# Kernel tuning notes

Measured on AMD Instinct MI355X. Metric: run time of the kernel, lower is better.

Reference implementation:

```python
import jax, jax.numpy as jnp
import numpy as np

B, N, E, F, OUT = 2, 50000, 150000, 256, 256

def setup_inputs() -> dict:
    key = jax.random.key(0)
    ks = jax.random.split(key, 8)
    X = jax.random.normal(ks[0], (B, N, F), dtype=jnp.float32)
    e = jax.random.uniform(ks[1], (B, E), dtype=jnp.float32)
    ri_idx = jax.random.randint(ks[2], (B, E), 0, N, dtype=jnp.int32)
    ro_idx = jax.random.randint(ks[3], (B, E), 0, N, dtype=jnp.int32)
    W1 = jax.random.normal(ks[4], (3 * F, OUT), dtype=jnp.float32) * (1.0 / np.sqrt(3 * F))
    b1 = jnp.zeros((OUT,), dtype=jnp.float32)
    W2 = jax.random.normal(ks[5], (OUT, OUT), dtype=jnp.float32) * (1.0 / np.sqrt(OUT))
    b2 = jnp.zeros((OUT,), dtype=jnp.float32)
    return {"X": X, "e": e, "ri_idx": ri_idx, "ro_idx": ro_idx,
            "W1": W1, "b1": b1, "W2": W2, "b2": b2}


def _aggregate(x, ew, ri, ro):
    # x: [N,F], ew: [E], ri/ro: [E] receiver/sender node ids per edge.
    # bi = Ri^T X = x[ri]; bo = Ro^T X = x[ro]
    # mi = Ri diag(e) bo : scatter-add weighted sender feats to receivers
    # mo = Ro diag(e) bi : scatter-add weighted receiver feats to senders
    n = x.shape[0]
    w = ew[:, None]
    mi = jax.ops.segment_sum(w * x[ro], ri, num_segments=n)
    mo = jax.ops.segment_sum(w * x[ri], ro, num_segments=n)
    return mi, mo


def reference(X, e, ri_idx, ro_idx, W1, b1, W2, b2):
    mi, mo = jax.vmap(_aggregate)(X, e, ri_idx, ro_idx)   # each [B,N,F]
    M = jnp.concatenate([mi, mo, X], axis=2)              # [B,N,3F]
    h = jnp.tanh(M @ W1 + b1)
    return jnp.tanh(h @ W2 + b2)
```

## Files before the change

### kernel.cpp

```cpp
#include <hip/hip_runtime.h>
#include <hip/hip_bf16.h>
#include <cstdint>
#include <cstddef>

#define BATCH 2
#define NNODE 50000
#define NEDGE 150000
#define FDIM 256
#define MTOT (BATCH * NNODE)
#define NSEG (2 * BATCH * NNODE)
#define NEDG2 (2 * BATCH * NEDGE)
#define SCAN_NB 98

typedef __attribute__((ext_vector_type(8))) __bf16 bf16x8;
typedef __attribute__((ext_vector_type(4))) float f32x4;

__device__ __forceinline__ ushort f32_to_bf16_rne(float x) {
    uint32_t u = __builtin_bit_cast(uint32_t, x);
    u = (u + 0x7fffu + ((u >> 16) & 1u)) >> 16;
    return (ushort)u;
}

__device__ __forceinline__ void split2(float x, ushort& h, ushort& l) {
    h = f32_to_bf16_rne(x);
    float hf = __builtin_bit_cast(float, ((uint32_t)h) << 16);
    l = f32_to_bf16_rne(x - hf);
}

__global__ __launch_bounds__(256)
void prep_kernel(const float* __restrict__ W1, const float* __restrict__ W2,
                 ushort* __restrict__ W1h, ushort* __restrict__ W1l,
                 ushort* __restrict__ W2h, ushort* __restrict__ W2l) {
    int idx = blockIdx.x * 256 + threadIdx.x;
    if (idx < 768 * 256) {
        int k = idx >> 8, n = idx & 255;
        ushort h, l;
        split2(W1[idx], h, l);
        W1h[n * 768 + k] = h;
        W1l[n * 768 + k] = l;
    }
    if (idx < 256 * 256) {
        int k = idx >> 8, n = idx & 255;
        ushort h, l;
        split2(W2[idx], h, l);
        W2h[n * 256 + k] = h;
        W2l[n * 256 + k] = l;
    }
}

__global__ __launch_bounds__(256)
void hist_kernel(const int* __restrict__ ri, const int* __restrict__ ro,
                 int* __restrict__ cnt) {
    int j = blockIdx.x * 256 + threadIdx.x;
    if (j >= BATCH * NEDGE) return;
    int b = j / NEDGE;
    atomicAdd(&cnt[(0 * BATCH + b) * NNODE + ri[j]], 1);
    atomicAdd(&cnt[(1 * BATCH + b) * NNODE + ro[j]], 1);
}

__global__ __launch_bounds__(256)
void scan1_kernel(const int* __restrict__ cnt, int* __restrict__ rs,
                  int* __restrict__ bsum) {
    __shared__ int s[256];
    int tid = threadIdx.x;
    int base = blockIdx.x * 2048 + tid * 8;
    int v[8];
    int loc = 0;
#pragma unroll
    for (int j = 0; j < 8; ++j) {
        int idx = base + j;
        int x = (idx < NSEG) ? cnt[idx] : 0;
        v[j] = x;
        loc += x;
    }
    s[tid] = loc;
    __syncthreads();
    for (int off = 1; off < 256; off <<= 1) {
        int t = (tid >= off) ? s[tid - off] : 0;
        __syncthreads();
        s[tid] += t;
        __syncthreads();
    }
    int run = (tid == 0) ? 0 : s[tid - 1];
#pragma unroll
    for (int j = 0; j < 8; ++j) {
        int idx = base + j;
        if (idx < NSEG) rs[idx] = run;
        run += v[j];
    }
    if (tid == 255) bsum[blockIdx.x] = s[255];
}

__global__ __launch_bounds__(128)
void scan2_kernel(int* __restrict__ bsum) {
    __shared__ int s[128];
    int tid = threadIdx.x;
    int x = (tid < SCAN_NB) ? bsum[tid] : 0;
    s[tid] = x;
    __syncthreads();
    for (int off = 1; off < 128; off <<= 1) {
        int t = (tid >= off) ? s[tid - off] : 0;
        __syncthreads();
        s[tid] += t;
        __syncthreads();
    }
    int ex = (tid == 0) ? 0 : s[tid - 1];
    if (tid < SCAN_NB) bsum[tid] = ex;
}

__global__ __launch_bounds__(256)
void scan3_kernel(int* __restrict__ rs, int* __restrict__ cur,
                  const int* __restrict__ bsum) {
    int base = blockIdx.x * 2048 + threadIdx.x * 8;
    int off = bsum[blockIdx.x];
#pragma unroll
    for (int j = 0; j < 8; ++j) {
        int idx = base + j;
        if (idx < NSEG) {
            int v = rs[idx] + off;
            rs[idx] = v;
            cur[idx] = v;
        }
    }
}

__global__ __launch_bounds__(256)
void fill_kernel(const int* __restrict__ ri, const int* __restrict__ ro,
                 const float* __restrict__ e, int* __restrict__ cur,
                 int* __restrict__ pidx, float* __restrict__ pw) {
    int j = blockIdx.x * 256 + threadIdx.x;
    if (j >= BATCH * NEDGE) return;
    int b = j / NEDGE;
    int vri = ri[j], vro = ro[j];
    float ew = e[j];
    int p0 = atomicAdd(&cur[(0 * BATCH + b) * NNODE + vri], 1);
    pidx[p0] = vro;
    pw[p0] = ew;
    int p1 = atomicAdd(&cur[(1 * BATCH + b) * NNODE + vro], 1);
    pidx[p1] = vri;
    pw[p1] = ew;
}

__global__ __launch_bounds__(256)
void gather_kernel(const float* __restrict__ X, const int* __restrict__ rs,
                   const int* __restrict__ cnt, const int* __restrict__ pidx,
                   const float* __restrict__ pw,
                   float* __restrict__ mi, float* __restrict__ mo) {
    int gid = blockIdx.x * 256 + threadIdx.x;
    int w = gid >> 6;
    int lane = gid & 63;
    if (w >= NSEG) return;
    int t = w / (BATCH * NNODE);
    int r = w - t * (BATCH * NNODE);
    int b = r / NNODE;
    int start = rs[w];
    int c = cnt[w];
    const float* Xb = X + (size_t)b * NNODE * FDIM;
    float4 acc = make_float4(0.f, 0.f, 0.f, 0.f);
    for (int i = 0; i < c; ++i) {
        int v = pidx[start + i];
        float ww = pw[start + i];
        float4 xv = *(const float4*)(Xb + (size_t)v * FDIM + lane * 4);
        acc.x += ww * xv.x;
        acc.y += ww * xv.y;
        acc.z += ww * xv.z;
        acc.w += ww * xv.w;
    }
    float* dst = (t == 0 ? mi : mo) + (size_t)r * FDIM + lane * 4;
    *(float4*)dst = acc;
}

template<int KTOT, bool SECOND>
__global__ __launch_bounds__(256, 2)
void gemm_kernel(const float* __restrict__ A0, const float* __restrict__ A1,
                 const float* __restrict__ A2,
                 const ushort* __restrict__ Bhg, const ushort* __restrict__ Blg,
                 const float* __restrict__ bias,
                 uint32_t* __restrict__ hout, float* __restrict__ fout) {
    __shared__ ushort Ah[128][36], Al[128][36], Bh[128][36], Bl[128][36];

    int tid = threadIdx.x;
    int lane = tid & 63;
    int wid = tid >> 6;
    int wm = wid >> 1, wn = wid & 1;
    int r0 = blockIdx.x * 128;
    int c0 = blockIdx.y * 128;

    f32x4 acc[4][4];
    f32x4 zero4 = {0.f, 0.f, 0.f, 0.f};
#pragma unroll
    for (int m = 0; m < 4; ++m)
#pragma unroll
        for (int n = 0; n < 4; ++n) acc[m][n] = zero4;

    for (int k0 = 0; k0 < KTOT; k0 += 32) {
        {
            int c4 = (tid & 7) * 4;
            int rr = tid >> 3;
            if constexpr (!SECOND) {
                const float* src;
                int kb;
                if (k0 < 256)      { src = A0; kb = k0; }
                else if (k0 < 512) { src = A1; kb = k0 - 256; }
                else               { src = A2; kb = k0 - 512; }
#pragma unroll
                for (int it = 0; it < 4; ++it) {
                    int row = it * 32 + rr;
                    int rg = r0 + row;
                    float4 v = make_float4(0.f, 0.f, 0.f, 0.f);
                    if (rg < MTOT) v = *(const float4*)(src + (size_t)rg * 256 + kb + c4);
                    ushort h0, l0, h1, l1, h2, l2, h3, l3;
                    split2(v.x, h0, l0); split2(v.y, h1, l1);
                    split2(v.z, h2, l2); split2(v.w, h3, l3);
                    *(ushort4*)&Ah[row][c4] = make_ushort4(h0, h1, h2, h3);
                    *(ushort4*)&Al[row][c4] = make_ushort4(l0, l1, l2, l3);
                }
            } else {
                const uint32_t* src = (const uint32_t*)A0;
#pragma unroll
                for (int it = 0; it < 4; ++it) {
                    int row = it * 32 + rr;
                    int rg = r0 + row;
                    uint4 v = make_uint4(0u, 0u, 0u, 0u);
                    if (rg < MTOT) v = *(const uint4*)(src + (size_t)rg * 256 + k0 + c4);
                    *(ushort4*)&Ah[row][c4] = make_ushort4((ushort)v.x, (ushort)v.y,
                                                           (ushort)v.z, (ushort)v.w);
                    *(ushort4*)&Al[row][c4] = make_ushort4((ushort)(v.x >> 16), (ushort)(v.y >> 16),
                                                           (ushort)(v.z >> 16), (ushort)(v.w >> 16));
                }
            }
        }
        {
            int i = tid & 127;
            int seg = (tid >> 7) * 16;
            const ushort* gh = Bhg + (size_t)(c0 + i) * KTOT + k0 + seg;
            const ushort* gl = Blg + (size_t)(c0 + i) * KTOT + k0 + seg;
#pragma unroll
            for (int j = 0; j < 2; ++j) {
                *(uint4*)&Bh[i][seg + j * 8] = *(const uint4*)(gh + j * 8);
                *(uint4*)&Bl[i][seg + j * 8] = *(const uint4*)(gl + j * 8);
            }
        }
        __syncthreads();

        {
            int ko = (lane >> 4) * 8;
            bf16x8 ah[4], al[4], bh[4], bl[4];
#pragma unroll
            for (int m = 0; m < 4; ++m) {
                int row = wm * 64 + m * 16 + (lane & 15);
                ah[m] = *(const bf16x8*)&Ah[row][ko];
                al[m] = *(const bf16x8*)&Al[row][ko];
            }
#pragma unroll
            for (int n = 0; n < 4; ++n) {
                int coln = wn * 64 + n * 16 + (lane & 15);
                bh[n] = *(const bf16x8*)&Bh[coln][ko];
                bl[n] = *(const bf16x8*)&Bl[coln][ko];
            }
#pragma unroll
            for (int m = 0; m < 4; ++m)
#pragma unroll
                for (int n = 0; n < 4; ++n) {
                    acc[m][n] = __builtin_amdgcn_mfma_f32_16x16x32_bf16(ah[m], bh[n], acc[m][n], 0, 0, 0);
                    acc[m][n] = __builtin_amdgcn_mfma_f32_16x16x32_bf16(al[m], bh[n], acc[m][n], 0, 0, 0);
                    acc[m][n] = __builtin_amdgcn_mfma_f32_16x16x32_bf16(ah[m], bl[n], acc[m][n], 0, 0, 0);
                }
        }
        __syncthreads();
    }

#pragma unroll
    for (int m = 0; m < 4; ++m) {
        int rbase = r0 + wm * 64 + m * 16 + ((lane >> 4) * 4);
#pragma unroll
        for (int n = 0; n < 4; ++n) {
            int col = c0 + wn * 64 + n * 16 + (lane & 15);
            float bv = bias[col];
#pragma unroll
            for (int q = 0; q < 4; ++q) {
                int row = rbase + q;
                if (row < MTOT) {
                    float t = tanhf(acc[m][n][q] + bv);
                    if constexpr (!SECOND) {
                        ushort h, l;
                        split2(t, h, l);
                        hout[(size_t)row * 256 + col] = (uint32_t)h | ((uint32_t)l << 16);
                    } else {
                        fout[(size_t)row * 256 + col] = t;
                    }
                }
            }
        }
    }
}

extern "C" void kernel_launch(void* const* d_in, const int* in_sizes, int n_in,
                              void* d_out, int out_size, void* d_ws, size_t ws_size,
                              hipStream_t stream) {
    const float* X  = (const float*)d_in[0];
    const float* e  = (const float*)d_in[1];
    const int*   ri = (const int*)d_in[2];
    const int*   ro = (const int*)d_in[3];
    const float* W1 = (const float*)d_in[4];
    const float* b1 = (const float*)d_in[5];
    const float* W2 = (const float*)d_in[6];
    const float* b2 = (const float*)d_in[7];
    float* out = (float*)d_out;

    char* ws = (char*)d_ws;
    const size_t szMI = (size_t)MTOT * 256 * 4;
    float*    mi   = (float*)ws;
    float*    mo   = (float*)(ws + szMI);
    char*     hreg = ws + 2 * szMI;
    uint32_t* hbuf = (uint32_t*)hreg;
    ushort*   W1h  = (ushort*)(ws + 3 * szMI);
    ushort*   W1l  = W1h + 768 * 256;
    ushort*   W2h  = W1l + 768 * 256;
    ushort*   W2l  = W2h + 256 * 256;

    int*   cnt  = (int*)(hreg);
    int*   rs   = (int*)(hreg + 800000);
    int*   cur  = (int*)(hreg + 1600000);
    int*   bsum = (int*)(hreg + 2400000);
    int*   pidx = (int*)(hreg + 2404096);
    float* pw   = (float*)(hreg + 4804096);

    hipMemsetAsync(cnt, 0, (size_t)NSEG * 4, stream);

    prep_kernel<<<768, 256, 0, stream>>>(W1, W2, W1h, W1l, W2h, W2l);

    hist_kernel<<<(BATCH * NEDGE + 255) / 256, 256, 0, stream>>>(ri, ro, cnt);
    scan1_kernel<<<SCAN_NB, 256, 0, stream>>>(cnt, rs, bsum);
    scan2_kernel<<<1, 128, 0, stream>>>(bsum);
    scan3_kernel<<<SCAN_NB, 256, 0, stream>>>(rs, cur, bsum);
    fill_kernel<<<(BATCH * NEDGE + 255) / 256, 256, 0, stream>>>(ri, ro, e, cur, pidx, pw);

    gather_kernel<<<NSEG / 4, 256, 0, stream>>>(X, rs, cnt, pidx, pw, mi, mo);

    dim3 grid1((MTOT + 127) / 128, 2);
    gemm_kernel<768, false><<<grid1, 256, 0, stream>>>(
        mi, mo, X, W1h, W1l, b1, hbuf, nullptr);

    gemm_kernel<256, true><<<grid1, 256, 0, stream>>>(
        (const float*)hbuf, nullptr, nullptr, W2h, W2l, b2, nullptr, out);
}
```

Before: 827.1 us.

## Double-buffer GEMM tiles via direct global-to-LDS loads with swizzled weight images

The GEMM kernels now stage A and B tiles straight into LDS with global_load_lds into a 64KB double buffer, prefetching the next K-tile while MFMAs run on the current one. The bf16 hi/lo split of A moves from the staging step to the fragment-read step, and the weights are pre-split into a swizzled tile-major image so B loads are contiguous and LDS reads avoid bank conflicts. The gather loop is also unrolled by two to keep more loads in flight. In exchange, each block uses much more LDS, which may cut occupancy, and the split work is repeated for each wave column.

```diff
diff --git a/kernel.cpp b/kernel.cpp
--- a/kernel.cpp
+++ b/kernel.cpp
@@ -9,11 +9,15 @@
 #define FDIM 256
 #define MTOT (BATCH * NNODE)
 #define NSEG (2 * BATCH * NNODE)
-#define NEDG2 (2 * BATCH * NEDGE)
 #define SCAN_NB 98
 
 typedef __attribute__((ext_vector_type(8))) __bf16 bf16x8;
+typedef __attribute__((ext_vector_type(8))) ushort u16x8;
 typedef __attribute__((ext_vector_type(4))) float f32x4;
+typedef __attribute__((ext_vector_type(4))) uint32_t u32x4;
+
+typedef const __attribute__((address_space(1))) uint32_t* gptr_t;
+typedef __attribute__((address_space(3))) uint32_t* lptr_t;
 
 __device__ __forceinline__ ushort f32_to_bf16_rne(float x) {
     uint32_t u = __builtin_bit_cast(uint32_t, x);
@@ -29,22 +33,40 @@
 
 __global__ __launch_bounds__(256)
 void prep_kernel(const float* __restrict__ W1, const float* __restrict__ W2,
-                 ushort* __restrict__ W1h, ushort* __restrict__ W1l,
-                 ushort* __restrict__ W2h, ushort* __restrict__ W2l) {
+                 ushort* __restrict__ i1h, ushort* __restrict__ i1l,
+                 ushort* __restrict__ i2h, ushort* __restrict__ i2l) {
     int idx = blockIdx.x * 256 + threadIdx.x;
-    if (idx < 768 * 256) {
-        int k = idx >> 8, n = idx & 255;
-        ushort h, l;
-        split2(W1[idx], h, l);
-        W1h[n * 768 + k] = h;
-        W1l[n * 768 + k] = l;
-    }
-    if (idx < 256 * 256) {
-        int k = idx >> 8, n = idx & 255;
-        ushort h, l;
-        split2(W2[idx], h, l);
-        W2h[n * 256 + k] = h;
-        W2l[n * 256 + k] = l;
+    if (idx < 24576) {
+        int kb = idx >> 10;
+        int col = (idx >> 2) & 255;
+        int s = idx & 3;
+        int cb = col >> 7, c = col & 127;
+        int sw = s ^ ((c >> 1) & 3);
+        ushort hs[8], ls[8];
+#pragma unroll
+        for (int j = 0; j < 8; ++j) {
+            int k = kb * 32 + sw * 8 + j;
+            split2(W1[(size_t)k * 256 + col], hs[j], ls[j]);
+        }
+        size_t off = ((size_t)(kb * 2 + cb) * 128 + c) * 32 + s * 8;
+#pragma unroll
+        for (int j = 0; j < 8; ++j) { i1h[off + j] = hs[j]; i1l[off + j] = ls[j]; }
+    }
+    if (idx < 8192) {
+        int kb = idx >> 10;
+        int col = (idx >> 2) & 255;
+        int s = idx & 3;
+        int cb = col >> 7, c = col & 127;
+        int sw = s ^ ((c >> 1) & 3);
+        ushort hs[8], ls[8];
+#pragma unroll
+        for (int j = 0; j < 8; ++j) {
+            int k = kb * 32 + sw * 8 + j;
+            split2(W2[(size_t)k * 256 + col], hs[j], ls[j]);
+        }
+        size_t off = ((size_t)(kb * 2 + cb) * 128 + c) * 32 + s * 8;
+#pragma unroll
+        for (int j = 0; j < 8; ++j) { i2h[off + j] = hs[j]; i2l[off + j] = ls[j]; }
     }
 }
 
@@ -155,36 +177,49 @@
     int b = r / NNODE;
     int start = rs[w];
     int c = cnt[w];
-    const float* Xb = X + (size_t)b * NNODE * FDIM;
+    int end = start + c;
+    const float* Xb = X + (size_t)b * NNODE * FDIM + lane * 4;
     float4 acc = make_float4(0.f, 0.f, 0.f, 0.f);
-    for (int i = 0; i < c; ++i) {
-        int v = pidx[start + i];
-        float ww = pw[start + i];
-        float4 xv = *(const float4*)(Xb + (size_t)v * FDIM + lane * 4);
-        acc.x += ww * xv.x;
-        acc.y += ww * xv.y;
-        acc.z += ww * xv.z;
-        acc.w += ww * xv.w;
+    int i = start;
+    for (; i + 1 < end; i += 2) {
+        int v0 = pidx[i], v1 = pidx[i + 1];
+        float w0 = pw[i], w1 = pw[i + 1];
+        float4 x0 = *(const float4*)(Xb + (size_t)v0 * FDIM);
+        float4 x1 = *(const float4*)(Xb + (size_t)v1 * FDIM);
+        acc.x += w0 * x0.x + w1 * x1.x;
+        acc.y += w0 * x0.y + w1 * x1.y;
+        acc.z += w0 * x0.z + w1 * x1.z;
+        acc.w += w0 * x0.w + w1 * x1.w;
+    }
+    if (i < end) {
+        int v0 = pidx[i];
+        float w0 = pw[i];
+        float4 x0 = *(const float4*)(Xb + (size_t)v0 * FDIM);
+        acc.x += w0 * x0.x;
+        acc.y += w0 * x0.y;
+        acc.z += w0 * x0.z;
+        acc.w += w0 * x0.w;
     }
     float* dst = (t == 0 ? mi : mo) + (size_t)r * FDIM + lane * 4;
     *(float4*)dst = acc;
 }
 
-template<int KTOT, bool SECOND>
+template<int NT, int AMODE>
 __global__ __launch_bounds__(256, 2)
 void gemm_kernel(const float* __restrict__ A0, const float* __restrict__ A1,
                  const float* __restrict__ A2,
-                 const ushort* __restrict__ Bhg, const ushort* __restrict__ Blg,
+                 const ushort* __restrict__ Bh_img, const ushort* __restrict__ Bl_img,
                  const float* __restrict__ bias,
                  uint32_t* __restrict__ hout, float* __restrict__ fout) {
-    __shared__ ushort Ah[128][36], Al[128][36], Bh[128][36], Bl[128][36];
+    __shared__ char smem[65536];
 
     int tid = threadIdx.x;
     int lane = tid & 63;
-    int wid = tid >> 6;
-    int wm = wid >> 1, wn = wid & 1;
+    int w = tid >> 6;
+    int wm = w >> 1, wn = w & 1;
     int r0 = blockIdx.x * 128;
-    int c0 = blockIdx.y * 128;
+    int cb = blockIdx.y;
+    int c0 = cb * 128;
 
     f32x4 acc[4][4];
     f32x4 zero4 = {0.f, 0.f, 0.f, 0.f};
@@ -193,81 +228,109 @@
 #pragma unroll
         for (int n = 0; n < 4; ++n) acc[m][n] = zero4;
 
-    for (int k0 = 0; k0 < KTOT; k0 += 32) {
-        {
-            int c4 = (tid & 7) * 4;
-            int rr = tid >> 3;
-            if constexpr (!SECOND) {
-                const float* src;
-                int kb;
-                if (k0 < 256)      { src = A0; kb = k0; }
-                else if (k0 < 512) { src = A1; kb = k0 - 256; }
-                else               { src = A2; kb = k0 - 512; }
-#pragma unroll
-                for (int it = 0; it < 4; ++it) {
-                    int row = it * 32 + rr;
-                    int rg = r0 + row;
-                    float4 v = make_float4(0.f, 0.f, 0.f, 0.f);
-                    if (rg < MTOT) v = *(const float4*)(src + (size_t)rg * 256 + kb + c4);
-                    ushort h0, l0, h1, l1, h2, l2, h3, l3;
-                    split2(v.x, h0, l0); split2(v.y, h1, l1);
-                    split2(v.z, h2, l2); split2(v.w, h3, l3);
-                    *(ushort4*)&Ah[row][c4] = make_ushort4(h0, h1, h2, h3);
-                    *(ushort4*)&Al[row][c4] = make_ushort4(l0, l1, l2, l3);
+    auto stage = [&](int buf, int t) {
+        const char* asrc;
+        int kb;
+        if constexpr (AMODE == 0) {
+            if (t < 8)       { asrc = (const char*)A0; kb = t * 128; }
+            else if (t < 16) { asrc = (const char*)A1; kb = (t - 8) * 128; }
+            else             { asrc = (const char*)A2; kb = (t - 16) * 128; }
+        } else {
+            asrc = (const char*)A0; kb = t * 128;
+        }
+        char* abase = smem + buf * 16384;
+#pragma unroll
+        for (int i = 0; i < 4; ++i) {
+            int inst = w * 4 + i;
+            int row = inst * 8 + (lane >> 3);
+            int rowg = r0 + row;
+            if (rowg > MTOT - 1) rowg = MTOT - 1;
+            int slot = (lane & 7) ^ (row & 7);
+            const char* g = asrc + (size_t)rowg * 1024 + kb + slot * 16;
+            __builtin_amdgcn_global_load_lds((gptr_t)g, (lptr_t)(abase + inst * 1024), 16, 0, 0);
+        }
+        int blk = t * 2 + cb;
+        const ushort* sh = Bh_img + (size_t)blk * 4096;
+        const ushort* sl = Bl_img + (size_t)blk * 4096;
+        char* bhbase = smem + 32768 + buf * 16384;
+        char* blbase = bhbase + 8192;
+#pragma unroll
+        for (int j = 0; j < 2; ++j) {
+            int inst = w * 2 + j;
+            __builtin_amdgcn_global_load_lds((gptr_t)(sh + inst * 512 + lane * 8),
+                                             (lptr_t)(bhbase + inst * 1024), 16, 0, 0);
+            __builtin_amdgcn_global_load_lds((gptr_t)(sl + inst * 512 + lane * 8),
+                                             (lptr_t)(blbase + inst * 1024), 16, 0, 0);
+        }
+    };
+
+    stage(0, 0);
+    asm volatile("s_waitcnt vmcnt(0)" ::: "memory");
+    __builtin_amdgcn_s_barrier();
+
+    int cur = 0;
+    for (int t = 0; t < NT; ++t) {
+        if (t + 1 < NT) stage(cur ^ 1, t + 1);
+
+        char* abase = smem + cur * 16384;
+        char* bhbase = smem + 32768 + cur * 16384;
+        char* blbase = bhbase + 8192;
+
+        bf16x8 ah[4], al[4], bh[4], bl[4];
+        int q0 = (lane >> 4) * 2;
+#pragma unroll
+        for (int m = 0; m < 4; ++m) {
+            int row = wm * 64 + m * 16 + (lane & 15);
+            const char* rp = abase + row * 128;
+            if constexpr (AMODE == 0) {
+                f32x4 lo = *(const f32x4*)(rp + ((q0) ^ (row & 7)) * 16);
+                f32x4 hi = *(const f32x4*)(rp + ((q0 + 1) ^ (row & 7)) * 16);
+                float v[8] = {lo[0], lo[1], lo[2], lo[3], hi[0], hi[1], hi[2], hi[3]};
+                u16x8 hv, lv;
+#pragma unroll
+                for (int j = 0; j < 8; ++j) {
+                    ushort hh, ll;
+                    split2(v[j], hh, ll);
+                    hv[j] = hh;
+                    lv[j] = ll;
                 }
+                ah[m] = __builtin_bit_cast(bf16x8, hv);
+                al[m] = __builtin_bit_cast(bf16x8, lv);
             } else {
-                const uint32_t* src = (const uint32_t*)A0;
-#pragma unroll
-                for (int it = 0; it < 4; ++it) {
-                    int row = it * 32 + rr;
-                    int rg = r0 + row;
-                    uint4 v = make_uint4(0u, 0u, 0u, 0u);
-                    if (rg < MTOT) v = *(const uint4*)(src + (size_t)rg * 256 + k0 + c4);
-                    *(ushort4*)&Ah[row][c4] = make_ushort4((ushort)v.x, (ushort)v.y,
-                                                           (ushort)v.z, (ushort)v.w);
-                    *(ushort4*)&Al[row][c4] = make_ushort4((ushort)(v.x >> 16), (ushort)(v.y >> 16),
-                                                           (ushort)(v.z >> 16), (ushort)(v.w >> 16));
+                u32x4 lo = *(const u32x4*)(rp + ((q0) ^ (row & 7)) * 16);
+                u32x4 hi = *(const u32x4*)(rp + ((q0 + 1) ^ (row & 7)) * 16);
+                u16x8 hv, lv;
+#pragma unroll
+                for (int j = 0; j < 4; ++j) {
+                    hv[j] = (ushort)lo[j];
+                    lv[j] = (ushort)(lo[j] >> 16);
+                    hv[j + 4] = (ushort)hi[j];
+                    lv[j + 4] = (ushort)(hi[j] >> 16);
                 }
+                ah[m] = __builtin_bit_cast(bf16x8, hv);
+                al[m] = __builtin_bit_cast(bf16x8, lv);
             }
         }
-        {
-            int i = tid & 127;
-            int seg = (tid >> 7) * 16;
-            const ushort* gh = Bhg + (size_t)(c0 + i) * KTOT + k0 + seg;
-            const ushort* gl = Blg + (size_t)(c0 + i) * KTOT + k0 + seg;
-#pragma unroll
-            for (int j = 0; j < 2; ++j) {
-                *(uint4*)&Bh[i][seg + j * 8] = *(const uint4*)(gh + j * 8);
-                *(uint4*)&Bl[i][seg + j * 8] = *(const uint4*)(gl + j * 8);
+        int ks = lane >> 4;
+#pragma unroll
+        for (int n = 0; n < 4; ++n) {
+            int c = wn * 64 + n * 16 + (lane & 15);
+            int so = (ks ^ ((c >> 1) & 3)) * 16;
+            bh[n] = *(const bf16x8*)(bhbase + c * 64 + so);
+            bl[n] = *(const bf16x8*)(blbase + c * 64 + so);
+        }
+#pragma unroll
+        for (int m = 0; m < 4; ++m)
+#pragma unroll
+            for (int n = 0; n < 4; ++n) {
+                acc[m][n] = __builtin_amdgcn_mfma_f32_16x16x32_bf16(ah[m], bh[n], acc[m][n], 0, 0, 0);
+                acc[m][n] = __builtin_amdgcn_mfma_f32_16x16x32_bf16(al[m], bh[n], acc[m][n], 0, 0, 0);
+                acc[m][n] = __builtin_amdgcn_mfma_f32_16x16x32_bf16(ah[m], bl[n], acc[m][n], 0, 0, 0);
             }
-        }
-        __syncthreads();
-
-        {
-            int ko = (lane >> 4) * 8;
-            bf16x8 ah[4], al[4], bh[4], bl[4];
-#pragma unroll
-            for (int m = 0; m < 4; ++m) {
-                int row = wm * 64 + m * 16 + (lane & 15);
-                ah[m] = *(const bf16x8*)&Ah[row][ko];
-                al[m] = *(const bf16x8*)&Al[row][ko];
-            }
-#pragma unroll
-            for (int n = 0; n < 4; ++n) {
-                int coln = wn * 64 + n * 16 + (lane & 15);
-                bh[n] = *(const bf16x8*)&Bh[coln][ko];
-                bl[n] = *(const bf16x8*)&Bl[coln][ko];
-            }
-#pragma unroll
-            for (int m = 0; m < 4; ++m)
-#pragma unroll
-                for (int n = 0; n < 4; ++n) {
-                    acc[m][n] = __builtin_amdgcn_mfma_f32_16x16x32_bf16(ah[m], bh[n], acc[m][n], 0, 0, 0);
-                    acc[m][n] = __builtin_amdgcn_mfma_f32_16x16x32_bf16(al[m], bh[n], acc[m][n], 0, 0, 0);
-                    acc[m][n] = __builtin_amdgcn_mfma_f32_16x16x32_bf16(ah[m], bl[n], acc[m][n], 0, 0, 0);
-                }
-        }
-        __syncthreads();
+
+        asm volatile("s_waitcnt vmcnt(0)" ::: "memory");
+        __builtin_amdgcn_s_barrier();
+        cur ^= 1;
     }
 
 #pragma unroll
@@ -281,13 +344,13 @@
             for (int q = 0; q < 4; ++q) {
                 int row = rbase + q;
                 if (row < MTOT) {
-                    float t = tanhf(acc[m][n][q] + bv);
-                    if constexpr (!SECOND) {
+                    float tv = tanhf(acc[m][n][q] + bv);
+                    if constexpr (AMODE == 0) {
                         ushort h, l;
-                        split2(t, h, l);
+                        split2(tv, h, l);
                         hout[(size_t)row * 256 + col] = (uint32_t)h | ((uint32_t)l << 16);
                     } else {
-                        fout[(size_t)row * 256 + col] = t;
+                        fout[(size_t)row * 256 + col] = tv;
                     }
                 }
             }
@@ -314,10 +377,10 @@
     float*    mo   = (float*)(ws + szMI);
     char*     hreg = ws + 2 * szMI;
     uint32_t* hbuf = (uint32_t*)hreg;
-    ushort*   W1h  = (ushort*)(ws + 3 * szMI);
-    ushort*   W1l  = W1h + 768 * 256;
-    ushort*   W2h  = W1l + 768 * 256;
-    ushort*   W2l  = W2h + 256 * 256;
+    ushort*   i1h  = (ushort*)(ws + 3 * szMI);
+    ushort*   i1l  = i1h + 196608;
+    ushort*   i2h  = i1l + 196608;
+    ushort*   i2l  = i2h + 65536;
 
     int*   cnt  = (int*)(hreg);
     int*   rs   = (int*)(hreg + 800000);
@@ -328,7 +391,7 @@
 
     hipMemsetAsync(cnt, 0, (size_t)NSEG * 4, stream);
 
-    prep_kernel<<<768, 256, 0, stream>>>(W1, W2, W1h, W1l, W2h, W2l);
+    prep_kernel<<<96, 256, 0, stream>>>(W1, W2, i1h, i1l, i2h, i2l);
 
     hist_kernel<<<(BATCH * NEDGE + 255) / 256, 256, 0, stream>>>(ri, ro, cnt);
     scan1_kernel<<<SCAN_NB, 256, 0, stream>>>(cnt, rs, bsum);
@@ -339,9 +402,9 @@
     gather_kernel<<<NSEG / 4, 256, 0, stream>>>(X, rs, cnt, pidx, pw, mi, mo);
 
     dim3 grid1((MTOT + 127) / 128, 2);
-    gemm_kernel<768, false><<<grid1, 256, 0, stream>>>(
-        mi, mo, X, W1h, W1l, b1, hbuf, nullptr);
-
-    gemm_kernel<256, true><<<grid1, 256, 0, stream>>>(
-        (const float*)hbuf, nullptr, nullptr, W2h, W2l, b2, nullptr, out);
-}
+    gemm_kernel<24, 0><<<grid1, 256, 0, stream>>>(
+        mi, mo, X, i1h, i1l, b1, hbuf, nullptr);
+
+    gemm_kernel<8, 1><<<grid1, 256, 0, stream>>>(
+        (const float*)hbuf, nullptr, nullptr, i2h, i2l, b2, nullptr, out);
+}
```

Result: faster. 676.3 us (-18.2%).
